# Performance work log

Measured on AMD Instinct MI355X. Metric: run time of the kernel, lower is better.

Reference implementation:

```python
import jax, jax.numpy as jnp
import numpy as np

# ---- module constants (kernel is hardcoded in scattering.__init__) ----
V_NODES = 2048
D_F = 128
J = 8              # filter-bank size (scaling + wavelets j=2..J)
L_LAYERS = 2       # scattering depth
R = 3.0
K = 1
DCOEF = (0.5, 0.5)
LAMB_MAX = 2.0
A = R * float(np.log(LAMB_MAX)) / (J - R + 1)  # kernel.a


def setup_inputs() -> dict:
    key = jax.random.key(0)
    kW, kf = jax.random.split(key)
    Araw = jax.random.uniform(kW, (V_NODES, V_NODES), dtype=jnp.float32)
    # symmetric adjacency with row sums ~0.9 (<1): distinct eigenvalues, wavelets active
    W = (Araw + Araw.T) * (0.9 / V_NODES)
    f = jax.random.normal(kf, (V_NODES, D_F), dtype=jnp.float32)
    return {"W": W, "f": f}


def _g_hat(x):
    # vectorized kernel.g_hat: sum_k d[k] cos(2*pi*k*(x/A + 0.5)) on (-A, 0], else 0
    d = jnp.asarray(DCOEF, dtype=x.dtype)
    ks = jnp.arange(K + 1, dtype=x.dtype)
    val = jnp.sum(d * jnp.cos(2.0 * jnp.pi * ks * (x[..., None] / A + 0.5)), axis=-1)
    return jnp.where((x > -A) & (x <= 0.0), val, 0.0)


def _filter_responses(E):
    # E: [V] eigenvalues -> [J, V] responses (row 0 = scaling, rows 1.. = wavelets j=2..J)
    js = jnp.arange(2, J + 1, dtype=E.dtype)                      # [J-1]
    wav = _g_hat(jnp.log(E)[None, :] - A * (js[:, None] - 1.0) / R)  # [J-1, V]
    d = jnp.asarray(DCOEF, dtype=E.dtype)
    s = (R / 2.0) * jnp.sum(d ** 2) + (R / 2.0) * d[0] ** 2 - jnp.sum(wav ** 2, axis=0)
    scal = jnp.sqrt(jnp.maximum(s, 0.0))                          # kernel.scaling
    return jnp.concatenate([scal[None, :], wav], axis=0)          # [J, V]


def reference(W, f):
    # compute_spectrum: NOTE source builds L = D (degrees only, no -W) then normalizes
    deg = W.sum(1)                                   # [V]
    dhalf = 1.0 / jnp.sqrt(jnp.maximum(1.0, deg))    # diag of D^{-1/2} with clamp
    Lmat = jnp.diag(deg) * dhalf[:, None] * dhalf[None, :]
    E, Vv = jnp.linalg.eigh(Lmat)
    E = jnp.abs(E)
    lam = _filter_responses(E)                       # [J, V]
    # filtering matrices g_j = V diag(lam_j) V^T, all j at once
    g = jnp.einsum('ai,ji,bi->jab', Vv, lam, Vv)     # [J, V, V]
    parts = [f.mean(0)]                              # S starts as f.mean(0)
    U = f[None]                                      # [1, V, d_f]
    for _ in range(L_LAYERS):
        # loop order in source: for f_ in U: for g_j in g -> index (u, j), u-major
        U = jnp.abs(jnp.einsum('jvw,uwd->ujvd', g, U)).reshape(-1, V_NODES, D_F)
        parts.append(U.mean(1).reshape(-1))          # concat of per-branch means
    return jnp.concatenate(parts)                    # [d_f*(1+J+J^2)]
```

## Files before the change

### kernel.cpp

```cpp
#include <hip/hip_runtime.h>
#include <math.h>

#define V 2048
#define DF 128
#define NK 73
#define NSLICE 16
#define A_F 0.34657359027997264f
#define TWO_PI_F 6.283185307179586f

__global__ __launch_bounds__(256) void k_filters(const float* __restrict__ W,
                                                 float* __restrict__ c) {
    __shared__ float red[4];
    const int v = blockIdx.x;
    const int tid = threadIdx.x;
    const float4* row = (const float4*)(W + (size_t)v * V);
    float4 a = row[tid];
    float4 b = row[tid + 256];
    float s = ((a.x + a.y) + (a.z + a.w)) + ((b.x + b.y) + (b.z + b.w));
    #pragma unroll
    for (int off = 32; off > 0; off >>= 1) s += __shfl_down(s, off, 64);
    if ((tid & 63) == 0) red[tid >> 6] = s;
    __syncthreads();
    if (tid == 0) {
        float deg = (red[0] + red[1]) + (red[2] + red[3]);
        float e = fabsf(deg / fmaxf(1.0f, deg));
        float x = logf(e);
        float sumsq = 0.0f;
        float wav[7];
        #pragma unroll
        for (int j = 2; j <= 8; ++j) {
            float t = x - A_F * (float)(j - 1) * (1.0f / 3.0f);
            float val = 0.0f;
            if (t > -A_F && t <= 0.0f) {
                val = 0.5f + 0.5f * cosf(TWO_PI_F * (t / A_F + 0.5f));
            }
            wav[j - 2] = val;
            sumsq += val * val;
        }
        c[v] = sqrtf(fmaxf(1.125f - sumsq, 0.0f));
        #pragma unroll
        for (int j = 0; j < 7; ++j) c[(j + 1) * V + v] = wav[j];
    }
}

__global__ __launch_bounds__(128) void k_scatter(const float* __restrict__ f,
                                                 const float* __restrict__ c,
                                                 float* __restrict__ part) {
    const int k = blockIdx.x;
    const int sl = blockIdx.y;
    const int d = threadIdx.x;
    const int v0 = sl * (V / NSLICE);
    const int v1 = v0 + (V / NSLICE);
    float acc = 0.0f;
    if (k == 0) {
        #pragma unroll 8
        for (int v = v0; v < v1; ++v)
            acc += f[(size_t)v * DF + d];
    } else if (k <= 8) {
        const float* cj = c + (k - 1) * V;
        #pragma unroll 8
        for (int v = v0; v < v1; ++v)
            acc += cj[v] * fabsf(f[(size_t)v * DF + d]);
    } else {
        const float* c1 = c + ((k - 9) >> 3) * V;
        const float* c2 = c + ((k - 9) & 7) * V;
        #pragma unroll 8
        for (int v = v0; v < v1; ++v)
            acc += c1[v] * c2[v] * fabsf(f[(size_t)v * DF + d]);
    }
    part[((size_t)sl * NK + k) * DF + d] = acc;
}

__global__ __launch_bounds__(256) void k_reduce(const float* __restrict__ part,
                                               float* __restrict__ out) {
    const int i = blockIdx.x * 256 + threadIdx.x;
    if (i < NK * DF) {
        float s = 0.0f;
        #pragma unroll
        for (int sl = 0; sl < NSLICE; ++sl) s += part[(size_t)sl * NK * DF + i];
        out[i] = s * (1.0f / (float)V);
    }
}

extern "C" void kernel_launch(void* const* d_in, const int* in_sizes, int n_in,
                              void* d_out, int out_size, void* d_ws, size_t ws_size,
                              hipStream_t stream) {
    const float* W = (const float*)d_in[0];
    const float* f = (const float*)d_in[1];
    float* out = (float*)d_out;

    float* c = (float*)d_ws;
    float* part = c + 8 * V;

    k_filters<<<V, 256, 0, stream>>>(W, c);
    k_scatter<<<dim3(NK, NSLICE), DF, 0, stream>>>(f, c, part);
    k_reduce<<<(NK * DF + 255) / 256, 256, 0, stream>>>(part, out);
}
```

Baseline: 74.88 us.

## Fuse degree, filter and scatter stages into one kernel with atomic accumulation

Replaces the three-kernel pipeline (filters, sliced scatter, reduce) with a zero kernel plus one fused kernel. Each block computes degrees and filter coefficients for 8 rows, then accumulates all 73 output channels in registers for those rows and adds them into the output with atomics. This removes the intermediate coefficient and partial-sum buffers and one launch, and reads f only once. In exchange it holds 73 accumulators per thread, which raises register pressure, and issues 256 blocks' worth of atomic adds on 9344 outputs, which adds contention and makes the summation order nondeterministic.

Measured after the change: 80.07 us. 6.9% more time.

```diff
diff --git a/kernel.cpp b/kernel.cpp
--- a/kernel.cpp
+++ b/kernel.cpp
@@ -4,81 +4,95 @@
 #define V 2048
 #define DF 128
 #define NK 73
-#define NSLICE 16
+#define RPB 8
+#define NB (V / RPB)
 #define A_F 0.34657359027997264f
 #define TWO_PI_F 6.283185307179586f
 
-__global__ __launch_bounds__(256) void k_filters(const float* __restrict__ W,
-                                                 float* __restrict__ c) {
-    __shared__ float red[4];
-    const int v = blockIdx.x;
-    const int tid = threadIdx.x;
-    const float4* row = (const float4*)(W + (size_t)v * V);
-    float4 a = row[tid];
-    float4 b = row[tid + 256];
-    float s = ((a.x + a.y) + (a.z + a.w)) + ((b.x + b.y) + (b.z + b.w));
+__global__ __launch_bounds__(256) void k_zero(float* __restrict__ out) {
+    int i = blockIdx.x * 256 + threadIdx.x;
+    if (i < NK * DF) out[i] = 0.0f;
+}
+
+__global__ __launch_bounds__(256) void k_fused(const float* __restrict__ W,
+                                               const float* __restrict__ f,
+                                               float* __restrict__ out) {
+    __shared__ float degs[RPB];
+    __shared__ float cl[8][RPB];
+    __shared__ float red[NK * DF];
+    const int tid  = threadIdx.x;
+    const int wave = tid >> 6, lane = tid & 63;
+    const int v0   = blockIdx.x * RPB;
+
     #pragma unroll
-    for (int off = 32; off > 0; off >>= 1) s += __shfl_down(s, off, 64);
-    if ((tid & 63) == 0) red[tid >> 6] = s;
+    for (int rr = 0; rr < 2; ++rr) {
+        const int vloc = wave * 2 + rr;
+        const float4* row = (const float4*)(W + (size_t)(v0 + vloc) * V);
+        float s = 0.0f;
+        #pragma unroll
+        for (int k = 0; k < 8; ++k) {
+            float4 a = row[lane + 64 * k];
+            s += (a.x + a.y) + (a.z + a.w);
+        }
+        #pragma unroll
+        for (int off = 32; off > 0; off >>= 1) s += __shfl_xor(s, off, 64);
+        if (lane == 0) degs[vloc] = s;
+    }
     __syncthreads();
-    if (tid == 0) {
-        float deg = (red[0] + red[1]) + (red[2] + red[3]);
+
+    if (tid < RPB) {
+        float deg = degs[tid];
         float e = fabsf(deg / fmaxf(1.0f, deg));
         float x = logf(e);
-        float sumsq = 0.0f;
-        float wav[7];
+        float sumsq = 0.0f, wv[7];
         #pragma unroll
         for (int j = 2; j <= 8; ++j) {
             float t = x - A_F * (float)(j - 1) * (1.0f / 3.0f);
             float val = 0.0f;
-            if (t > -A_F && t <= 0.0f) {
+            if (t > -A_F && t <= 0.0f)
                 val = 0.5f + 0.5f * cosf(TWO_PI_F * (t / A_F + 0.5f));
-            }
-            wav[j - 2] = val;
+            wv[j - 2] = val;
             sumsq += val * val;
         }
-        c[v] = sqrtf(fmaxf(1.125f - sumsq, 0.0f));
+        cl[0][tid] = sqrtf(fmaxf(1.125f - sumsq, 0.0f));
         #pragma unroll
-        for (int j = 0; j < 7; ++j) c[(j + 1) * V + v] = wav[j];
+        for (int j = 0; j < 7; ++j) cl[j + 1][tid] = wv[j];
     }
-}
+    __syncthreads();
 
-__global__ __launch_bounds__(128) void k_scatter(const float* __restrict__ f,
-                                                 const float* __restrict__ c,
-                                                 float* __restrict__ part) {
-    const int k = blockIdx.x;
-    const int sl = blockIdx.y;
-    const int d = threadIdx.x;
-    const int v0 = sl * (V / NSLICE);
-    const int v1 = v0 + (V / NSLICE);
-    float acc = 0.0f;
-    if (k == 0) {
-        #pragma unroll 8
-        for (int v = v0; v < v1; ++v)
-            acc += f[(size_t)v * DF + d];
-    } else if (k <= 8) {
-        const float* cj = c + (k - 1) * V;
-        #pragma unroll 8
-        for (int v = v0; v < v1; ++v)
-            acc += cj[v] * fabsf(f[(size_t)v * DF + d]);
-    } else {
-        const float* c1 = c + ((k - 9) >> 3) * V;
-        const float* c2 = c + ((k - 9) & 7) * V;
-        #pragma unroll 8
-        for (int v = v0; v < v1; ++v)
-            acc += c1[v] * c2[v] * fabsf(f[(size_t)v * DF + d]);
+    const int rep = tid >> 7;
+    const int d   = tid & 127;
+    float acc[NK];
+    #pragma unroll
+    for (int k = 0; k < NK; ++k) acc[k] = 0.0f;
+    #pragma unroll
+    for (int i = 0; i < 4; ++i) {
+        const int vloc = rep * 4 + i;
+        float fv = f[(size_t)(v0 + vloc) * DF + d];
+        float af = fabsf(fv);
+        float cj[8];
+        #pragma unroll
+        for (int j = 0; j < 8; ++j) cj[j] = cl[j][vloc];
+        acc[0] += fv;
+        float tu[8];
+        #pragma unroll
+        for (int u = 0; u < 8; ++u) { tu[u] = cj[u] * af; acc[1 + u] += tu[u]; }
+        #pragma unroll
+        for (int u = 0; u < 8; ++u)
+            #pragma unroll
+            for (int j = 0; j < 8; ++j)
+                acc[9 + u * 8 + j] += tu[u] * cj[j];
     }
-    part[((size_t)sl * NK + k) * DF + d] = acc;
-}
 
-__global__ __launch_bounds__(256) void k_reduce(const float* __restrict__ part,
-                                               float* __restrict__ out) {
-    const int i = blockIdx.x * 256 + threadIdx.x;
-    if (i < NK * DF) {
-        float s = 0.0f;
+    if (rep == 1) {
         #pragma unroll
-        for (int sl = 0; sl < NSLICE; ++sl) s += part[(size_t)sl * NK * DF + i];
-        out[i] = s * (1.0f / (float)V);
+        for (int k = 0; k < NK; ++k) red[k * DF + d] = acc[k];
+    }
+    __syncthreads();
+    if (rep == 0) {
+        #pragma unroll
+        for (int k = 0; k < NK; ++k)
+            atomicAdd(&out[k * DF + d], (acc[k] + red[k * DF + d]) * (1.0f / (float)V));
     }
 }
 
@@ -89,10 +103,6 @@
     const float* f = (const float*)d_in[1];
     float* out = (float*)d_out;
 
-    float* c = (float*)d_ws;
-    float* part = c + 8 * V;
-
-    k_filters<<<V, 256, 0, stream>>>(W, c);
-    k_scatter<<<dim3(NK, NSLICE), DF, 0, stream>>>(f, c, part);
-    k_reduce<<<(NK * DF + 255) / 256, 256, 0, stream>>>(part, out);
+    k_zero<<<(NK * DF + 255) / 256, 256, 0, stream>>>(out);
+    k_fused<<<NB, 256, 0, stream>>>(W, f, out);
 }
```
